# Optimization experiments

Hardware: AMD Instinct MI355X
Metric: run time of the kernel (lower is better)

The kernel has to match this reference:

```python
import jax, jax.numpy as jnp
import numpy as np

NEG_SLOPE = 0.2
MASK_VAL = -9e15

def _xavier_uniform(key, shape, gain=1.414):
    fan_in, fan_out = shape[0], shape[1]
    limit = gain * np.sqrt(6.0 / (fan_in + fan_out))
    return jax.random.uniform(key, shape, jnp.float32, -limit, limit)

def setup_inputs() -> dict:
    key = jax.random.key(0)
    k1, k2, k3, k4 = jax.random.split(key, 4)
    N, D_IN, D_OUT = 8192, 256, 64
    inp = jax.random.normal(k1, (1, N, D_IN), jnp.float32)
    adj = jax.random.randint(k2, (N, N), 0, 2, jnp.int32)
    w = _xavier_uniform(k3, (D_IN, D_OUT))
    a = _xavier_uniform(k4, (2 * D_OUT, 1))
    return {"input": inp, "adj": adj, "w": w, "a": a}

def reference(input, adj, w, a):
    # h = X @ W  -> [N, D_out]
    h = input[0] @ w
    D = h.shape[1]
    # e_ij = leakyrelu([h_i || h_j] @ a) = leakyrelu(h_i @ a[:D] + h_j @ a[D:])
    # avoids materializing the N*N x 2D concat tensor; same math as the original.
    src = h @ a[:D, 0]   # [N]
    dst = h @ a[D:, 0]   # [N]
    e = jax.nn.leaky_relu(src[:, None] + dst[None, :], NEG_SLOPE)  # [N, N]
    att = jnp.where(adj > 0, e, MASK_VAL)
    att = jax.nn.softmax(att, axis=1)
    # dropout p=0.0 / eval mode -> identity
    h_prime = att @ h  # [N, D_out]
    return jax.nn.elu(h_prime)  # concat=True -> elu
```

## Files before the change

### kernel.cpp

```cpp
#include <hip/hip_runtime.h>
#include <hip/hip_bf16.h>

#define NN 8192
#define DIN 256
#define DOUT 64
#define NCH 8
#define CHJ (NN / NCH)

typedef __attribute__((ext_vector_type(4))) float f32x4;
typedef __attribute__((ext_vector_type(4))) int i32x4;
typedef __attribute__((ext_vector_type(8))) short short8;

__device__ __forceinline__ unsigned short f2bf(float f) {
  unsigned u = __float_as_uint(f);
  u += 0x7fffu + ((u >> 16) & 1u);
  return (unsigned short)(u >> 16);
}
__device__ __forceinline__ unsigned pk2bf(float lo, float hi) {
  return (unsigned)f2bf(lo) | ((unsigned)f2bf(hi) << 16);
}
__device__ __forceinline__ unsigned cvtpk(float lo, float hi) {
  unsigned r;
  asm("v_cvt_pk_bf16_f32 %0, %1, %2" : "=v"(r) : "v"(lo), "v"(hi));
  return r;
}

__global__ __launch_bounds__(256) void k_prep(const float* __restrict__ W,
                                              unsigned short* __restrict__ WTb) {
  const int i = blockIdx.x * 256 + threadIdx.x;
  const int d = i >> 8, k = i & 255;
  WTb[i] = f2bf(W[k * DOUT + d]);
}

__global__ __launch_bounds__(256) void k_hw(
    const float* __restrict__ X, const unsigned short* __restrict__ WTb,
    const float* __restrict__ A, float* __restrict__ src,
    float* __restrict__ dst, float* __restrict__ dmax_arr,
    unsigned short* __restrict__ HTt) {
  const int tid = threadIdx.x;
  const int wid = tid >> 6, lane = tid & 63;
  const int l15 = lane & 15, kc = lane >> 4;
  const int rt = blockIdx.x * 64 + wid * 16;
  const float* __restrict__ xr = X + (size_t)(rt + l15) * DIN + kc * 8;
  const unsigned short* __restrict__ wb = WTb + (size_t)l15 * DIN + kc * 8;
  f32x4 acc0 = {0.f, 0.f, 0.f, 0.f};
  f32x4 acc1 = acc0, acc2 = acc0, acc3 = acc0;
#pragma unroll
  for (int ks = 0; ks < 8; ++ks) {
    const f32x4 x0 = *(const f32x4*)(xr + ks * 32);
    const f32x4 x1 = *(const f32x4*)(xr + ks * 32 + 4);
    short8 af;
    ((unsigned*)&af)[0] = pk2bf(x0[0], x0[1]);
    ((unsigned*)&af)[1] = pk2bf(x0[2], x0[3]);
    ((unsigned*)&af)[2] = pk2bf(x1[0], x1[1]);
    ((unsigned*)&af)[3] = pk2bf(x1[2], x1[3]);
    const short8 b0 = *(const short8*)(wb + ks * 32);
    const short8 b1 = *(const short8*)(wb + 16 * DIN + ks * 32);
    const short8 b2 = *(const short8*)(wb + 32 * DIN + ks * 32);
    const short8 b3 = *(const short8*)(wb + 48 * DIN + ks * 32);
    acc0 = __builtin_amdgcn_mfma_f32_16x16x32_bf16(af, b0, acc0, 0, 0, 0);
    acc1 = __builtin_amdgcn_mfma_f32_16x16x32_bf16(af, b1, acc1, 0, 0, 0);
    acc2 = __builtin_amdgcn_mfma_f32_16x16x32_bf16(af, b2, acc2, 0, 0, 0);
    acc3 = __builtin_amdgcn_mfma_f32_16x16x32_bf16(af, b3, acc3, 0, 0, 0);
  }
  const float as0 = A[l15], as1 = A[16 + l15], as2 = A[32 + l15],
              as3 = A[48 + l15];
  const float ad0 = A[64 + l15], ad1 = A[80 + l15], ad2 = A[96 + l15],
              ad3 = A[112 + l15];
  float dm = -1e30f;
#pragma unroll
  for (int v = 0; v < 4; ++v) {
    float sv = acc0[v] * as0 + acc1[v] * as1 + acc2[v] * as2 + acc3[v] * as3;
    float dv = acc0[v] * ad0 + acc1[v] * ad1 + acc2[v] * ad2 + acc3[v] * ad3;
#pragma unroll
    for (int m = 1; m < 16; m <<= 1) {
      sv += __shfl_xor(sv, m);
      dv += __shfl_xor(dv, m);
    }
    if (l15 == 0) {
      src[rt + kc * 4 + v] = sv;
      dst[rt + kc * 4 + v] = dv;
    }
    dm = fmaxf(dm, dv);
  }
  dm = fmaxf(dm, __shfl_xor(dm, 16));
  dm = fmaxf(dm, __shfl_xor(dm, 32));
  if (lane == 0) dmax_arr[blockIdx.x * 4 + wid] = dm;
  unsigned short* __restrict__ hs =
      HTt + (size_t)(rt >> 5) * 2048 + l15 * 32 + (rt & 16) + kc * 4;
  *(unsigned*)(hs + 0 * 512) = pk2bf(acc0[0], acc0[1]);
  *(unsigned*)(hs + 0 * 512 + 2) = pk2bf(acc0[2], acc0[3]);
  *(unsigned*)(hs + 1 * 512) = pk2bf(acc1[0], acc1[1]);
  *(unsigned*)(hs + 1 * 512 + 2) = pk2bf(acc1[2], acc1[3]);
  *(unsigned*)(hs + 2 * 512) = pk2bf(acc2[0], acc2[1]);
  *(unsigned*)(hs + 2 * 512 + 2) = pk2bf(acc2[2], acc2[3]);
  *(unsigned*)(hs + 3 * 512) = pk2bf(acc3[0], acc3[1]);
  *(unsigned*)(hs + 3 * 512 + 2) = pk2bf(acc3[2], acc3[3]);
}

__global__ __launch_bounds__(256) void k_att(
    const int* __restrict__ adj, const float* __restrict__ src,
    const float* __restrict__ dst, const float* __restrict__ dmax_arr,
    const unsigned short* __restrict__ HTt, float* __restrict__ pacc,
    float* __restrict__ ps) {
  __shared__ float E1s[CHJ], E2s[CHJ];
  __shared__ float dsm[4];
  __shared__ unsigned short Hs[16384];
  const int tid = threadIdx.x;
  const int wid = tid >> 6, lane = tid & 63;
  const int l15 = lane & 15, kc = lane >> 4;
  const int rowtile = blockIdx.x * 128 + wid * 32;
  const int c = blockIdx.y;
  const int cbase = c * CHJ;
  {
    const f32x4 dv4 = *(const f32x4*)(dst + cbase + tid * 4);
    E1s[tid * 4 + 0] = __expf(dv4[0]);
    E1s[tid * 4 + 1] = __expf(dv4[1]);
    E1s[tid * 4 + 2] = __expf(dv4[2]);
    E1s[tid * 4 + 3] = __expf(dv4[3]);
    E2s[tid * 4 + 0] = __expf(0.2f * dv4[0]);
    E2s[tid * 4 + 1] = __expf(0.2f * dv4[1]);
    E2s[tid * 4 + 2] = __expf(0.2f * dv4[2]);
    E2s[tid * 4 + 3] = __expf(0.2f * dv4[3]);
    float dm0 = fmaxf(dmax_arr[tid], dmax_arr[tid + 256]);
#pragma unroll
    for (int m = 1; m < 64; m <<= 1) dm0 = fmaxf(dm0, __shfl_xor(dm0, m));
    if (lane == 0) dsm[wid] = dm0;
  }
  __syncthreads();
  const float dmx = fmaxf(fmaxf(dsm[0], dsm[1]), fmaxf(dsm[2], dsm[3]));
  const int arA = rowtile + l15, arB = arA + 16;
  const float sA = src[arA], sB = src[arB];
  const float eA = sA + dmx, eB = sB + dmx;
  const float miA = fmaxf(eA, 0.2f * eA), miB = fmaxf(eB, 0.2f * eB);
  const float cA1 = __expf(sA - miA), cA2 = __expf(0.2f * sA - miA);
  const float cB1 = __expf(sB - miB), cB2 = __expf(0.2f * sB - miB);
  f32x4 aA0 = {0.f, 0.f, 0.f, 0.f};
  f32x4 aA1 = aA0, aA2 = aA0, aA3 = aA0;
  f32x4 aB0 = aA0, aB1 = aA0, aB2 = aA0, aB3 = aA0;
  float sacA = 0.f, sacB = 0.f;
  const unsigned short* __restrict__ Hsrc =
      HTt + (size_t)(cbase >> 5) * 2048 + (tid >> 6) * 512 + (tid & 15) * 32 +
      ((tid >> 4) & 3) * 8;
  const int HsW = (tid >> 6) * 512 + (tid & 63) * 8;
  const int hfirst = (blockIdx.x + blockIdx.y) & 3;
#pragma unroll
  for (int hh = 0; hh < 4; ++hh) {
    const int h = (hfirst + hh) & 3;
    unsigned loA[4], hiA[4], loB[4], hiB[4];
    {
      unsigned long long wA64[4] = {0ull, 0ull, 0ull, 0ull};
      unsigned long long wB64[4] = {0ull, 0ull, 0ull, 0ull};
      const int* __restrict__ ab =
          adj + (size_t)rowtile * NN + cbase + h * 256 + lane * 4;
#pragma unroll
      for (int g = 0; g < 4; ++g) {
        i32x4 v[8];
#pragma unroll
        for (int r8 = 0; r8 < 8; ++r8)
          v[r8] = *(const i32x4*)(ab + (size_t)(g * 8 + r8) * NN);
#pragma unroll
        for (int r8 = 0; r8 < 8; ++r8) {
          const int rr = g * 8 + r8;
          const unsigned long long b0 = __ballot(v[r8][0] > 0);
          const unsigned long long b1 = __ballot(v[r8][1] > 0);
          const unsigned long long b2 = __ballot(v[r8][2] > 0);
          const unsigned long long b3 = __ballot(v[r8][3] > 0);
          if (rr < 16) {
            const bool isA = (l15 == rr);
            wA64[0] = isA ? b0 : wA64[0];
            wA64[1] = isA ? b1 : wA64[1];
            wA64[2] = isA ? b2 : wA64[2];
            wA64[3] = isA ? b3 : wA64[3];
          } else {
            const bool isB = (l15 == rr - 16);
            wB64[0] = isB ? b0 : wB64[0];
            wB64[1] = isB ? b1 : wB64[1];
            wB64[2] = isB ? b2 : wB64[2];
            wB64[3] = isB ? b3 : wB64[3];
          }
        }
      }
#pragma unroll
      for (int m = 0; m < 4; ++m) {
        const unsigned long long shA = wA64[m] >> (kc * 2);
        const unsigned long long shB = wB64[m] >> (kc * 2);
        loA[m] = (unsigned)shA;
        hiA[m] = (unsigned)(shA >> 32);
        loB[m] = (unsigned)shB;
        hiB[m] = (unsigned)(shB >> 32);
      }
    }
    if (hh) __syncthreads();
#pragma unroll
    for (int it = 0; it < 8; ++it) {
      const short8 v = *(const short8*)(Hsrc + (h * 8 + it) * 2048);
      *(short8*)(Hs + it * 2048 + HsW) = v;
    }
    __syncthreads();
#pragma unroll
    for (int q = 0; q < 2; ++q) {
#pragma unroll 2
      for (int s4 = 0; s4 < 4; ++s4) {
        const int sl = q * 4 + s4;
        const int jr = (h * 8 + sl) * 32 + kc * 8;
        const f32x4 e1a = *(const f32x4*)&E1s[jr];
        const f32x4 e1b = *(const f32x4*)&E1s[jr + 4];
        const f32x4 e2a = *(const f32x4*)&E2s[jr];
        const f32x4 e2b = *(const f32x4*)&E2s[jr + 4];
        float pvA[8], pvB[8];
#pragma unroll
        for (int e = 0; e < 8; ++e) {
          const float E1v = (e < 4) ? e1a[e & 3] : e1b[e & 3];
          const float E2v = (e < 4) ? e2a[e & 3] : e2b[e & 3];
          const unsigned bsh = s4 * 8 + (e >> 2);
          const unsigned wa = q ? hiA[e & 3] : loA[e & 3];
          const unsigned wb2 = q ? hiB[e & 3] : loB[e & 3];
          float pA = fmaxf(cA1 * E1v, cA2 * E2v);
          float pB = fmaxf(cB1 * E1v, cB2 * E2v);
          pA = ((wa >> bsh) & 1u) ? pA : 0.f;
          pB = ((wb2 >> bsh) & 1u) ? pB : 0.f;
          sacA += pA;
          sacB += pB;
          pvA[e] = pA;
          pvB[e] = pB;
        }
        short8 afA, afB;
        ((unsigned*)&afA)[0] = cvtpk(pvA[0], pvA[1]);
        ((unsigned*)&afA)[1] = cvtpk(pvA[2], pvA[3]);
        ((unsigned*)&afA)[2] = cvtpk(pvA[4], pvA[5]);
        ((unsigned*)&afA)[3] = cvtpk(pvA[6], pvA[7]);
        ((unsigned*)&afB)[0] = cvtpk(pvB[0], pvB[1]);
        ((unsigned*)&afB)[1] = cvtpk(pvB[2], pvB[3]);
        ((unsigned*)&afB)[2] = cvtpk(pvB[4], pvB[5]);
        ((unsigned*)&afB)[3] = cvtpk(pvB[6], pvB[7]);
        const unsigned short* hj = Hs + sl * 2048 + lane * 8;
        const short8 bf0 = *(const short8*)(hj);
        const short8 bf1 = *(const short8*)(hj + 512);
        const short8 bf2 = *(const short8*)(hj + 1024);
        const short8 bf3 = *(const short8*)(hj + 1536);
        aA0 = __builtin_amdgcn_mfma_f32_16x16x32_bf16(afA, bf0, aA0, 0, 0, 0);
        aB0 = __builtin_amdgcn_mfma_f32_16x16x32_bf16(afB, bf0, aB0, 0, 0, 0);
        aA1 = __builtin_amdgcn_mfma_f32_16x16x32_bf16(afA, bf1, aA1, 0, 0, 0);
        aB1 = __builtin_amdgcn_mfma_f32_16x16x32_bf16(afB, bf1, aB1, 0, 0, 0);
        aA2 = __builtin_amdgcn_mfma_f32_16x16x32_bf16(afA, bf2, aA2, 0, 0, 0);
        aB2 = __builtin_amdgcn_mfma_f32_16x16x32_bf16(afB, bf2, aB2, 0, 0, 0);
        aA3 = __builtin_amdgcn_mfma_f32_16x16x32_bf16(afA, bf3, aA3, 0, 0, 0);
        aB3 = __builtin_amdgcn_mfma_f32_16x16x32_bf16(afB, bf3, aB3, 0, 0, 0);
      }
    }
  }
  float stA = sacA, stB = sacB;
  stA += __shfl_xor(stA, 16);
  stA += __shfl_xor(stA, 32);
  stB += __shfl_xor(stB, 16);
  stB += __shfl_xor(stB, 32);
  if (lane < 16) {
    ps[(size_t)c * NN + arA] = stA;
    ps[(size_t)c * NN + arB] = stB;
  }
  const int orA = rowtile + kc * 4;
  float* __restrict__ pbA = pacc + ((size_t)c * NN + orA) * DOUT + l15;
  float* __restrict__ pbB = pbA + (size_t)16 * DOUT;
#pragma unroll
  for (int v = 0; v < 4; ++v) {
    pbA[(size_t)v * DOUT + 0] = aA0[v];
    pbA[(size_t)v * DOUT + 16] = aA1[v];
    pbA[(size_t)v * DOUT + 32] = aA2[v];
    pbA[(size_t)v * DOUT + 48] = aA3[v];
    pbB[(size_t)v * DOUT + 0] = aB0[v];
    pbB[(size_t)v * DOUT + 16] = aB1[v];
    pbB[(size_t)v * DOUT + 32] = aB2[v];
    pbB[(size_t)v * DOUT + 48] = aB3[v];
  }
}

__global__ __launch_bounds__(256) void k_fin(const float* __restrict__ pacc,
                                             const float* __restrict__ ps,
                                             float* __restrict__ out) {
  const int idx4 = blockIdx.x * 256 + threadIdx.x;
  const int i = idx4 >> 4;
  float ss = 0.f;
  f32x4 as = {0.f, 0.f, 0.f, 0.f};
  const f32x4* __restrict__ p4 = (const f32x4*)pacc;
#pragma unroll
  for (int c = 0; c < NCH; ++c) {
    ss += ps[(size_t)c * NN + i];
    const f32x4 v = p4[(size_t)c * (NN * DOUT / 4) + idx4];
    as[0] += v[0];
    as[1] += v[1];
    as[2] += v[2];
    as[3] += v[3];
  }
  const float inv = 1.f / ss;
  f32x4 o;
#pragma unroll
  for (int e = 0; e < 4; ++e) {
    const float v = as[e] * inv;
    o[e] = v > 0.f ? v : (__expf(v) - 1.f);
  }
  *(f32x4*)(out + (size_t)idx4 * 4) = o;
}

extern "C" void kernel_launch(void* const* d_in, const int* in_sizes, int n_in,
                              void* d_out, int out_size, void* d_ws,
                              size_t ws_size, hipStream_t stream) {
  const float* X = (const float*)d_in[0];
  const int* adj = (const int*)d_in[1];
  const float* W = (const float*)d_in[2];
  const float* A = (const float*)d_in[3];
  float* out = (float*)d_out;
  char* ws = (char*)d_ws;
  float* src = (float*)(ws);
  float* dst = (float*)(ws + (32u << 10));
  float* dmax_arr = (float*)(ws + (64u << 10));
  unsigned short* WTb = (unsigned short*)(ws + (128u << 10));
  unsigned short* HTt = (unsigned short*)(ws + (256u << 10));
  float* pacc = (float*)(ws + (16u << 20));
  float* ps = pacc + (size_t)NCH * NN * DOUT;
  k_prep<<<64, 256, 0, stream>>>(W, WTb);
  k_hw<<<NN / 64, 256, 0, stream>>>(X, WTb, A, src, dst, dmax_arr, HTt);
  k_att<<<dim3(NN / 128, NCH), 256, 0, stream>>>(adj, src, dst, dmax_arr, HTt,
                                                 pacc, ps);
  k_fin<<<NN * DOUT / 1024, 256, 0, stream>>>(pacc, ps, out);
}
```

Before: 74.64 us.

## Software-pipeline adjacency loads for the next column slice behind MFMA compute

The adjacency loads and ballot mask construction for the next 256-column slice are now issued while the current slice's softmax-weight and MFMA steps run. The first slice's loads are issued before the exp table setup so their latency is hidden. Loads and ballots are interleaved with the compute steps so memory latency overlaps with math, since the kernel is dominated by streaming the int32 adjacency matrix. The cost is holding 32 prefetched i32x4 vectors live in registers, which may lower occupancy or cause spills.

```diff
diff --git a/kernel.cpp b/kernel.cpp
--- a/kernel.cpp
+++ b/kernel.cpp
@@ -112,6 +112,59 @@
   const int rowtile = blockIdx.x * 128 + wid * 32;
   const int c = blockIdx.y;
   const int cbase = c * CHJ;
+  const int hfirst = (blockIdx.x + blockIdx.y) & 3;
+  const int* __restrict__ abase = adj + (size_t)rowtile * NN + cbase + lane * 4;
+  i32x4 vb0[8], vb1[8], vb2[8], vb3[8];
+  unsigned long long nwA64[4] = {0ull, 0ull, 0ull, 0ull};
+  unsigned long long nwB64[4] = {0ull, 0ull, 0ull, 0ull};
+  unsigned loA[4], hiA[4], loB[4], hiB[4];
+
+#define ISSUE8(VB, G, H)                                                     \
+  do {                                                                       \
+    _Pragma("unroll") for (int r8 = 0; r8 < 8; ++r8) VB[r8] =                \
+        *(const i32x4*)(abase + (size_t)((G) * 8 + r8) * NN + (H) * 256);    \
+  } while (0)
+
+#define BALLOT8(VB, G)                                                       \
+  do {                                                                       \
+    _Pragma("unroll") for (int r8 = 0; r8 < 8; ++r8) {                       \
+      const int rr = (G) * 8 + r8;                                           \
+      const unsigned long long b0 = __ballot(VB[r8][0] > 0);                 \
+      const unsigned long long b1 = __ballot(VB[r8][1] > 0);                 \
+      const unsigned long long b2 = __ballot(VB[r8][2] > 0);                 \
+      const unsigned long long b3 = __ballot(VB[r8][3] > 0);                 \
+      if ((G) < 2) {                                                         \
+        const bool isA = (l15 == rr);                                        \
+        nwA64[0] = isA ? b0 : nwA64[0];                                      \
+        nwA64[1] = isA ? b1 : nwA64[1];                                      \
+        nwA64[2] = isA ? b2 : nwA64[2];                                      \
+        nwA64[3] = isA ? b3 : nwA64[3];                                      \
+      } else {                                                               \
+        const bool isB = (l15 == rr - 16);                                   \
+        nwB64[0] = isB ? b0 : nwB64[0];                                      \
+        nwB64[1] = isB ? b1 : nwB64[1];                                      \
+        nwB64[2] = isB ? b2 : nwB64[2];                                      \
+        nwB64[3] = isB ? b3 : nwB64[3];                                      \
+      }                                                                      \
+    }                                                                        \
+  } while (0)
+
+#define SHIFTMASKS                                                           \
+  do {                                                                       \
+    _Pragma("unroll") for (int m = 0; m < 4; ++m) {                          \
+      const unsigned long long shA = nwA64[m] >> (kc * 2);                   \
+      const unsigned long long shB = nwB64[m] >> (kc * 2);                   \
+      loA[m] = (unsigned)shA;                                                \
+      hiA[m] = (unsigned)(shA >> 32);                                        \
+      loB[m] = (unsigned)shB;                                                \
+      hiB[m] = (unsigned)(shB >> 32);                                        \
+    }                                                                        \
+  } while (0)
+
+  ISSUE8(vb0, 0, hfirst);
+  ISSUE8(vb1, 1, hfirst);
+  ISSUE8(vb2, 2, hfirst);
+  ISSUE8(vb3, 3, hfirst);
   {
     const f32x4 dv4 = *(const f32x4*)(dst + cbase + tid * 4);
     E1s[tid * 4 + 0] = __expf(dv4[0]);
@@ -135,6 +188,11 @@
   const float miA = fmaxf(eA, 0.2f * eA), miB = fmaxf(eB, 0.2f * eB);
   const float cA1 = __expf(sA - miA), cA2 = __expf(0.2f * sA - miA);
   const float cB1 = __expf(sB - miB), cB2 = __expf(0.2f * sB - miB);
+  BALLOT8(vb0, 0);
+  BALLOT8(vb1, 1);
+  BALLOT8(vb2, 2);
+  BALLOT8(vb3, 3);
+  SHIFTMASKS;
   f32x4 aA0 = {0.f, 0.f, 0.f, 0.f};
   f32x4 aA1 = aA0, aA2 = aA0, aA3 = aA0;
   f32x4 aB0 = aA0, aB1 = aA0, aB2 = aA0, aB3 = aA0;
@@ -143,54 +201,58 @@
       HTt + (size_t)(cbase >> 5) * 2048 + (tid >> 6) * 512 + (tid & 15) * 32 +
       ((tid >> 4) & 3) * 8;
   const int HsW = (tid >> 6) * 512 + (tid & 63) * 8;
-  const int hfirst = (blockIdx.x + blockIdx.y) & 3;
-#pragma unroll
+
+  auto cstep = [&](int h, int q, int s4) {
+    const int sl = q * 4 + s4;
+    const int jr = (h * 8 + sl) * 32 + kc * 8;
+    const f32x4 e1a = *(const f32x4*)&E1s[jr];
+    const f32x4 e1b = *(const f32x4*)&E1s[jr + 4];
+    const f32x4 e2a = *(const f32x4*)&E2s[jr];
+    const f32x4 e2b = *(const f32x4*)&E2s[jr + 4];
+    float pvA[8], pvB[8];
+#pragma unroll
+    for (int e = 0; e < 8; ++e) {
+      const float E1v = (e < 4) ? e1a[e & 3] : e1b[e & 3];
+      const float E2v = (e < 4) ? e2a[e & 3] : e2b[e & 3];
+      const unsigned bsh = s4 * 8 + (e >> 2);
+      const unsigned wa = q ? hiA[e & 3] : loA[e & 3];
+      const unsigned wb2 = q ? hiB[e & 3] : loB[e & 3];
+      float pA = fmaxf(cA1 * E1v, cA2 * E2v);
+      float pB = fmaxf(cB1 * E1v, cB2 * E2v);
+      pA = ((wa >> bsh) & 1u) ? pA : 0.f;
+      pB = ((wb2 >> bsh) & 1u) ? pB : 0.f;
+      sacA += pA;
+      sacB += pB;
+      pvA[e] = pA;
+      pvB[e] = pB;
+    }
+    short8 afA, afB;
+    ((unsigned*)&afA)[0] = cvtpk(pvA[0], pvA[1]);
+    ((unsigned*)&afA)[1] = cvtpk(pvA[2], pvA[3]);
+    ((unsigned*)&afA)[2] = cvtpk(pvA[4], pvA[5]);
+    ((unsigned*)&afA)[3] = cvtpk(pvA[6], pvA[7]);
+    ((unsigned*)&afB)[0] = cvtpk(pvB[0], pvB[1]);
+    ((unsigned*)&afB)[1] = cvtpk(pvB[2], pvB[3]);
+    ((unsigned*)&afB)[2] = cvtpk(pvB[4], pvB[5]);
+    ((unsigned*)&afB)[3] = cvtpk(pvB[6], pvB[7]);
+    const unsigned short* hj = Hs + sl * 2048 + lane * 8;
+    const short8 bf0 = *(const short8*)(hj);
+    const short8 bf1 = *(const short8*)(hj + 512);
+    const short8 bf2 = *(const short8*)(hj + 1024);
+    const short8 bf3 = *(const short8*)(hj + 1536);
+    aA0 = __builtin_amdgcn_mfma_f32_16x16x32_bf16(afA, bf0, aA0, 0, 0, 0);
+    aB0 = __builtin_amdgcn_mfma_f32_16x16x32_bf16(afB, bf0, aB0, 0, 0, 0);
+    aA1 = __builtin_amdgcn_mfma_f32_16x16x32_bf16(afA, bf1, aA1, 0, 0, 0);
+    aB1 = __builtin_amdgcn_mfma_f32_16x16x32_bf16(afB, bf1, aB1, 0, 0, 0);
+    aA2 = __builtin_amdgcn_mfma_f32_16x16x32_bf16(afA, bf2, aA2, 0, 0, 0);
+    aB2 = __builtin_amdgcn_mfma_f32_16x16x32_bf16(afB, bf2, aB2, 0, 0, 0);
+    aA3 = __builtin_amdgcn_mfma_f32_16x16x32_bf16(afA, bf3, aA3, 0, 0, 0);
+    aB3 = __builtin_amdgcn_mfma_f32_16x16x32_bf16(afB, bf3, aB3, 0, 0, 0);
+  };
+
   for (int hh = 0; hh < 4; ++hh) {
     const int h = (hfirst + hh) & 3;
-    unsigned loA[4], hiA[4], loB[4], hiB[4];
-    {
-      unsigned long long wA64[4] = {0ull, 0ull, 0ull, 0ull};
-      unsigned long long wB64[4] = {0ull, 0ull, 0ull, 0ull};
-      const int* __restrict__ ab =
-          adj + (size_t)rowtile * NN + cbase + h * 256 + lane * 4;
-#pragma unroll
-      for (int g = 0; g < 4; ++g) {
-        i32x4 v[8];
-#pragma unroll
-        for (int r8 = 0; r8 < 8; ++r8)
-          v[r8] = *(const i32x4*)(ab + (size_t)(g * 8 + r8) * NN);
-#pragma unroll
-        for (int r8 = 0; r8 < 8; ++r8) {
-          const int rr = g * 8 + r8;
-          const unsigned long long b0 = __ballot(v[r8][0] > 0);
-          const unsigned long long b1 = __ballot(v[r8][1] > 0);
-          const unsigned long long b2 = __ballot(v[r8][2] > 0);
-          const unsigned long long b3 = __ballot(v[r8][3] > 0);
-          if (rr < 16) {
-            const bool isA = (l15 == rr);
-            wA64[0] = isA ? b0 : wA64[0];
-            wA64[1] = isA ? b1 : wA64[1];
-            wA64[2] = isA ? b2 : wA64[2];
-            wA64[3] = isA ? b3 : wA64[3];
-          } else {
-            const bool isB = (l15 == rr - 16);
-            wB64[0] = isB ? b0 : wB64[0];
-            wB64[1] = isB ? b1 : wB64[1];
-            wB64[2] = isB ? b2 : wB64[2];
-            wB64[3] = isB ? b3 : wB64[3];
-          }
-        }
-      }
-#pragma unroll
-      for (int m = 0; m < 4; ++m) {
-        const unsigned long long shA = wA64[m] >> (kc * 2);
-        const unsigned long long shB = wB64[m] >> (kc * 2);
-        loA[m] = (unsigned)shA;
-        hiA[m] = (unsigned)(shA >> 32);
-        loB[m] = (unsigned)shB;
-        hiB[m] = (unsigned)(shB >> 32);
-      }
-    }
+    const int hn = (hfirst + hh + 1) & 3;
     if (hh) __syncthreads();
 #pragma unroll
     for (int it = 0; it < 8; ++it) {
@@ -198,58 +260,35 @@
       *(short8*)(Hs + it * 2048 + HsW) = v;
     }
     __syncthreads();
-#pragma unroll
-    for (int q = 0; q < 2; ++q) {
-#pragma unroll 2
-      for (int s4 = 0; s4 < 4; ++s4) {
-        const int sl = q * 4 + s4;
-        const int jr = (h * 8 + sl) * 32 + kc * 8;
-        const f32x4 e1a = *(const f32x4*)&E1s[jr];
-        const f32x4 e1b = *(const f32x4*)&E1s[jr + 4];
-        const f32x4 e2a = *(const f32x4*)&E2s[jr];
-        const f32x4 e2b = *(const f32x4*)&E2s[jr + 4];
-        float pvA[8], pvB[8];
-#pragma unroll
-        for (int e = 0; e < 8; ++e) {
-          const float E1v = (e < 4) ? e1a[e & 3] : e1b[e & 3];
-          const float E2v = (e < 4) ? e2a[e & 3] : e2b[e & 3];
-          const unsigned bsh = s4 * 8 + (e >> 2);
-          const unsigned wa = q ? hiA[e & 3] : loA[e & 3];
-          const unsigned wb2 = q ? hiB[e & 3] : loB[e & 3];
-          float pA = fmaxf(cA1 * E1v, cA2 * E2v);
-          float pB = fmaxf(cB1 * E1v, cB2 * E2v);
-          pA = ((wa >> bsh) & 1u) ? pA : 0.f;
-          pB = ((wb2 >> bsh) & 1u) ? pB : 0.f;
-          sacA += pA;
-          sacB += pB;
-          pvA[e] = pA;
-          pvB[e] = pB;
-        }
-        short8 afA, afB;
-        ((unsigned*)&afA)[0] = cvtpk(pvA[0], pvA[1]);
-        ((unsigned*)&afA)[1] = cvtpk(pvA[2], pvA[3]);
-        ((unsigned*)&afA)[2] = cvtpk(pvA[4], pvA[5]);
-        ((unsigned*)&afA)[3] = cvtpk(pvA[6], pvA[7]);
-        ((unsigned*)&afB)[0] = cvtpk(pvB[0], pvB[1]);
-        ((unsigned*)&afB)[1] = cvtpk(pvB[2], pvB[3]);
-        ((unsigned*)&afB)[2] = cvtpk(pvB[4], pvB[5]);
-        ((unsigned*)&afB)[3] = cvtpk(pvB[6], pvB[7]);
-        const unsigned short* hj = Hs + sl * 2048 + lane * 8;
-        const short8 bf0 = *(const short8*)(hj);
-        const short8 bf1 = *(const short8*)(hj + 512);
-        const short8 bf2 = *(const short8*)(hj + 1024);
-        const short8 bf3 = *(const short8*)(hj + 1536);
-        aA0 = __builtin_amdgcn_mfma_f32_16x16x32_bf16(afA, bf0, aA0, 0, 0, 0);
-        aB0 = __builtin_amdgcn_mfma_f32_16x16x32_bf16(afB, bf0, aB0, 0, 0, 0);
-        aA1 = __builtin_amdgcn_mfma_f32_16x16x32_bf16(afA, bf1, aA1, 0, 0, 0);
-        aB1 = __builtin_amdgcn_mfma_f32_16x16x32_bf16(afB, bf1, aB1, 0, 0, 0);
-        aA2 = __builtin_amdgcn_mfma_f32_16x16x32_bf16(afA, bf2, aA2, 0, 0, 0);
-        aB2 = __builtin_amdgcn_mfma_f32_16x16x32_bf16(afB, bf2, aB2, 0, 0, 0);
-        aA3 = __builtin_amdgcn_mfma_f32_16x16x32_bf16(afA, bf3, aA3, 0, 0, 0);
-        aB3 = __builtin_amdgcn_mfma_f32_16x16x32_bf16(afB, bf3, aB3, 0, 0, 0);
-      }
-    }
-  }
+    if (hh < 3) {
+      ISSUE8(vb0, 0, hn);
+      cstep(h, 0, 0);
+      ISSUE8(vb1, 1, hn);
+      cstep(h, 0, 1);
+      ISSUE8(vb2, 2, hn);
+      cstep(h, 0, 2);
+      ISSUE8(vb3, 3, hn);
+      cstep(h, 0, 3);
+      BALLOT8(vb0, 0);
+      cstep(h, 1, 0);
+      BALLOT8(vb1, 1);
+      cstep(h, 1, 1);
+      BALLOT8(vb2, 2);
+      cstep(h, 1, 2);
+      BALLOT8(vb3, 3);
+      cstep(h, 1, 3);
+      SHIFTMASKS;
+    } else {
+#pragma unroll
+      for (int q = 0; q < 2; ++q)
+#pragma unroll
+        for (int s4 = 0; s4 < 4; ++s4) cstep(h, q, s4);
+    }
+  }
+#undef ISSUE8
+#undef BALLOT8
+#undef SHIFTMASKS
+
   float stA = sacA, stB = sacB;
   stA += __shfl_xor(stA, 16);
   stA += __shfl_xor(stA, 32);
```

After: 85.94 us. 1.15x slower.
